# Kernel tuning notes

Measured on AMD Instinct MI355X. Metric: run time of the kernel, lower is better.

Reference implementation:

```python
import jax, jax.numpy as jnp
import numpy as np

B, S, D = 32, 512, 512
MAX_MEL = 2048
SLOWDOWN = 0.5


def setup_inputs() -> dict:
    key = jax.random.key(0)
    k1, k2 = jax.random.split(key)
    sequences = jax.random.normal(k1, (B, S, D), dtype=jnp.float32)
    # raw float durations in [0, 8); after +0.5 / clamp(min=1) / int cast -> 1..8
    durations = jax.random.uniform(k2, (B, S), dtype=jnp.float32) * 8.0
    return {"sequences": sequences, "durations": durations, "max_mel_length": MAX_MEL}


def reference(sequences, durations, max_mel_length):
    # durations = (durations + slowdown).clamp(min=1).int()  (truncation toward zero,
    # values are >= 1 so plain astype matches torch .int())
    d = jnp.maximum(durations + SLOWDOWN, 1.0).astype(jnp.int32)  # [B,S]
    csum = jnp.cumsum(d, axis=1)                                   # [B,S] end offsets
    t = jnp.arange(max_mel_length, dtype=jnp.int32)                # [T]
    # frame t belongs to token j = #(csum <= t) = searchsorted(csum, t, 'right')
    idx = jax.vmap(lambda c: jnp.searchsorted(c, t, side='right'))(csum)  # [B,T]
    valid = idx < d.shape[1]                                        # frames past total -> pad
    safe_idx = jnp.minimum(idx, d.shape[1] - 1)
    gathered = jnp.take_along_axis(sequences, safe_idx[..., None], axis=1)  # [B,T,D]
    padded = jnp.where(valid[..., None], gathered, jnp.zeros((), sequences.dtype))
    return padded, d
```

## Files before the change

kernel.cpp:

```cpp
#include <hip/hip_runtime.h>


#define BB 32
#define SS 512
#define DD 512
#define TT 2048
#define SLOWDOWN 0.5f
#define FPB 32

__global__ __launch_bounds__(SS)
void lr_scan_scatter(const float* __restrict__ durations,
                     float* __restrict__ d_out_tail,
                     int* __restrict__ frame_tok) {
    const int b    = blockIdx.x;
    const int tid  = threadIdx.x;
    const int lane = tid & 63;
    const int wv   = tid >> 6;

    int* ft = frame_tok + (size_t)b * TT;
#pragma unroll
    for (int i = 0; i < TT / SS; ++i) ft[tid + i * SS] = SS;

    float df = durations[b * SS + tid] + SLOWDOWN;
    df = fmaxf(df, 1.0f);
    int di = (int)df;
    d_out_tail[b * SS + tid] = (float)di;

    int v = di;
#pragma unroll
    for (int off = 1; off < 64; off <<= 1) {
        int n = __shfl_up(v, off);
        if (lane >= off) v += n;
    }
    __shared__ int wtot[8];
    if (lane == 63) wtot[wv] = v;
    __syncthreads();
    int woff = 0;
#pragma unroll
    for (int w = 0; w < 7; ++w) woff += (w < wv) ? wtot[w] : 0;

    const int csum  = v + woff;
    const int start = csum - di;
    if (start < TT) {
        const int end = (csum < TT) ? csum : TT;
        for (int f = start; f < end; ++f) ft[f] = tid;
    }
}

__global__ __launch_bounds__(256)
void lr_gather(const float* __restrict__ seq,
               const int* __restrict__ frame_tok,
               float* __restrict__ out) {
    const int tid   = threadIdx.x;
    const int fbase = blockIdx.x * FPB;
    __shared__ int stok[FPB];
    if (tid < FPB) stok[tid] = frame_tok[fbase + tid];
    __syncthreads();

    const int sub  = tid >> 7;
    const int lane = tid & 127;
    const int b    = fbase >> 11;
    const float* sbase = seq + (size_t)b * SS * DD;

#pragma unroll 4
    for (int p = 0; p < FPB / 2; ++p) {
        const int fi  = p * 2 + sub;
        const int tok = stok[fi];
        float4* o = reinterpret_cast<float4*>(out + (size_t)(fbase + fi) * DD);
        if (tok < SS) {
            const float4* s4 = reinterpret_cast<const float4*>(sbase + (size_t)tok * DD);
            o[lane] = s4[lane];
        } else {
            o[lane] = make_float4(0.f, 0.f, 0.f, 0.f);
        }
    }
}

extern "C" void kernel_launch(void* const* d_in, const int* in_sizes, int n_in,
                              void* d_out, int out_size, void* d_ws, size_t ws_size,
                              hipStream_t stream) {
    const float* sequences = (const float*)d_in[0];
    const float* durations = (const float*)d_in[1];

    float* out        = (float*)d_out;
    float* d_out_tail = out + (size_t)BB * TT * DD;
    int*   frame_tok  = (int*)d_ws;

    lr_scan_scatter<<<BB, SS, 0, stream>>>(durations, d_out_tail, frame_tok);
    lr_gather<<<(BB * TT) / FPB, 256, 0, stream>>>(sequences, frame_tok, out);
}
```

Measured before the change: 36.45 us.

## Fuse duration scan and gather into one kernel with per-block binary search

Merges the scan/scatter kernel and the gather kernel into a single launch. Each block recomputes the prefix sum of its batch's durations in shared memory, two tokens per thread, then binary-searches the frame-to-token index for its 32 frames. This removes the second kernel launch, the serial dependency between the kernels, and the workspace round trip for the frame-to-token map. In exchange, every block redundantly reads the durations and repeats the scan.

```diff
diff --git a/kernel.cpp b/kernel.cpp
--- a/kernel.cpp
+++ b/kernel.cpp
@@ -8,70 +8,75 @@
 #define SLOWDOWN 0.5f
 #define FPB 32
 
-__global__ __launch_bounds__(SS)
-void lr_scan_scatter(const float* __restrict__ durations,
-                     float* __restrict__ d_out_tail,
-                     int* __restrict__ frame_tok) {
-    const int b    = blockIdx.x;
-    const int tid  = threadIdx.x;
-    const int lane = tid & 63;
-    const int wv   = tid >> 6;
+__global__ __launch_bounds__(256)
+void lr_fused(const float* __restrict__ durations,
+              const float* __restrict__ seq,
+              float* __restrict__ out,
+              float* __restrict__ d_out_tail) {
+    const int blk   = blockIdx.x;
+    const int b     = blk >> 6;
+    const int chunk = blk & 63;
+    const int tbase = chunk * FPB;
+    const int tid   = threadIdx.x;
+    const int lane  = tid & 63;
+    const int wv    = tid >> 6;
 
-    int* ft = frame_tok + (size_t)b * TT;
-#pragma unroll
-    for (int i = 0; i < TT / SS; ++i) ft[tid + i * SS] = SS;
+    __shared__ int csum[SS];
+    __shared__ int wtot[4];
+    __shared__ int stok[FPB];
 
-    float df = durations[b * SS + tid] + SLOWDOWN;
-    df = fmaxf(df, 1.0f);
-    int di = (int)df;
-    d_out_tail[b * SS + tid] = (float)di;
+    const float2 dur = *reinterpret_cast<const float2*>(durations + b * SS + tid * 2);
+    const int d0 = (int)fmaxf(dur.x + SLOWDOWN, 1.0f);
+    const int d1 = (int)fmaxf(dur.y + SLOWDOWN, 1.0f);
 
-    int v = di;
+    int v = d0 + d1;
 #pragma unroll
     for (int off = 1; off < 64; off <<= 1) {
         int n = __shfl_up(v, off);
         if (lane >= off) v += n;
     }
-    __shared__ int wtot[8];
     if (lane == 63) wtot[wv] = v;
     __syncthreads();
     int woff = 0;
 #pragma unroll
-    for (int w = 0; w < 7; ++w) woff += (w < wv) ? wtot[w] : 0;
+    for (int w = 0; w < 3; ++w) woff += (w < wv) ? wtot[w] : 0;
 
-    const int csum  = v + woff;
-    const int start = csum - di;
-    if (start < TT) {
-        const int end = (csum < TT) ? csum : TT;
-        for (int f = start; f < end; ++f) ft[f] = tid;
+    const int c1 = v + woff;
+    csum[2 * tid]     = c1 - d1;
+    csum[2 * tid + 1] = c1;
+
+    if (chunk == 0) {
+        d_out_tail[b * SS + 2 * tid]     = (float)d0;
+        d_out_tail[b * SS + 2 * tid + 1] = (float)d1;
     }
-}
+    __syncthreads();
 
-__global__ __launch_bounds__(256)
-void lr_gather(const float* __restrict__ seq,
-               const int* __restrict__ frame_tok,
-               float* __restrict__ out) {
-    const int tid   = threadIdx.x;
-    const int fbase = blockIdx.x * FPB;
-    __shared__ int stok[FPB];
-    if (tid < FPB) stok[tid] = frame_tok[fbase + tid];
+    if (tid < FPB) {
+        const int t = tbase + tid;
+        int lo = 0, hi = SS;
+        while (lo < hi) {
+            const int mid = (lo + hi) >> 1;
+            if (csum[mid] <= t) lo = mid + 1; else hi = mid;
+        }
+        stok[tid] = lo;
+    }
     __syncthreads();
 
     const int sub  = tid >> 7;
-    const int lane = tid & 127;
-    const int b    = fbase >> 11;
+    const int l    = tid & 127;
     const float* sbase = seq + (size_t)b * SS * DD;
+    float* obase = out + ((size_t)b * TT + tbase) * DD;
 
 #pragma unroll 4
     for (int p = 0; p < FPB / 2; ++p) {
         const int fi  = p * 2 + sub;
         const int tok = stok[fi];
-        float4* o = reinterpret_cast<float4*>(out + (size_t)(fbase + fi) * DD);
+        float4* o = reinterpret_cast<float4*>(obase + (size_t)fi * DD);
         if (tok < SS) {
             const float4* s4 = reinterpret_cast<const float4*>(sbase + (size_t)tok * DD);
-            o[lane] = s4[lane];
+            o[l] = s4[l];
         } else {
-            o[lane] = make_float4(0.f, 0.f, 0.f, 0.f);
+            o[l] = make_float4(0.f, 0.f, 0.f, 0.f);
         }
     }
 }
@@ -84,8 +89,6 @@
 
     float* out        = (float*)d_out;
     float* d_out_tail = out + (size_t)BB * TT * DD;
-    int*   frame_tok  = (int*)d_ws;
 
-    lr_scan_scatter<<<BB, SS, 0, stream>>>(durations, d_out_tail, frame_tok);
-    lr_gather<<<(BB * TT) / FPB, 256, 0, stream>>>(sequences, frame_tok, out);
+    lr_fused<<<BB * (TT / FPB), 256, 0, stream>>>(durations, sequences, out, d_out_tail);
 }
```

Measured after the change: 32.44 us. -11.0%, faster.
